# Kernel optimization log

Measured on AMD Instinct MI355X. Metric: run time of the kernel, lower is better.

Reference implementation:

```python
import jax, jax.numpy as jnp
import numpy as np

N = 20000        # genes
E = 100000       # edges per relation
D_IN = 512
HID = 64         # hidden_dim (per-head channels in layers 0,1)
HEADS = 8
D_H = HID * HEADS   # 512 hidden width
D_OUT = 256
NEG_SLOPE = 0.2  # GATv2Conv default negative_slope


def _gatv2(x, src, dst, Wl, bl, Wr, br, att, out_bias, heads, ch):
    """PyG GATv2Conv, add_self_loops=False, concat=True, eval mode (no dropout)."""
    n = x.shape[0]
    xl = (x @ Wl + bl).reshape(n, heads, ch)   # lin_l (source transform)
    xr = (x @ Wr + br).reshape(n, heads, ch)   # lin_r (target transform)
    e = jax.nn.leaky_relu(xl[src] + xr[dst], NEG_SLOPE)   # [E,H,C]
    score = jnp.einsum('ehc,hc->eh', e, att)              # [E,H]
    # segment softmax over incoming edges of each destination node
    m = jax.ops.segment_max(score, dst, num_segments=n)   # [N,H]
    w = jnp.exp(score - m[dst])
    z = jax.ops.segment_sum(w, dst, num_segments=n)
    alpha = w / z[dst]
    out = jax.ops.segment_sum(alpha[:, :, None] * xl[src], dst, num_segments=n)
    return out.reshape(n, heads * ch) + out_bias


def _layernorm(x, g, b):
    mu = x.mean(-1, keepdims=True)
    var = x.var(-1, keepdims=True)
    return (x - mu) * jax.lax.rsqrt(var + 1e-5) * g + b


def setup_inputs() -> dict:
    key = jax.random.key(0)
    ks = jax.random.split(key, 12)
    gn = lambda k, shape, fan_in: (jax.random.normal(k, shape, dtype=jnp.float32)
                                   / np.float32(np.sqrt(fan_in)))
    inp = {}
    inp['x'] = jax.random.normal(ks[0], (N, D_IN), dtype=jnp.float32)
    inp['edge_index'] = jax.random.randint(ks[1], (3, 2, E), 0, N, dtype=jnp.int32)
    # input projection  Linear(512 -> 512)
    inp['proj_w'] = gn(ks[2], (D_IN, D_H), D_IN)
    inp['proj_b'] = jnp.zeros((D_H,), jnp.float32)
    # layers 0,1: stacked over [layer, edge_type]
    inp['l01_lin_l_w'] = gn(ks[3], (2, 3, D_H, D_H), D_H)
    inp['l01_lin_l_b'] = jnp.zeros((2, 3, D_H), jnp.float32)
    inp['l01_lin_r_w'] = gn(ks[4], (2, 3, D_H, D_H), D_H)
    inp['l01_lin_r_b'] = jnp.zeros((2, 3, D_H), jnp.float32)
    inp['l01_att'] = gn(ks[5], (2, 3, HEADS, HID), HID)
    inp['l01_bias'] = jnp.zeros((2, 3, D_H), jnp.float32)
    # layer 2: heads=1, out_channels=256, stacked over edge_type
    inp['l2_lin_l_w'] = gn(ks[6], (3, D_H, D_OUT), D_H)
    inp['l2_lin_l_b'] = jnp.zeros((3, D_OUT), jnp.float32)
    inp['l2_lin_r_w'] = gn(ks[7], (3, D_H, D_OUT), D_H)
    inp['l2_lin_r_b'] = jnp.zeros((3, D_OUT), jnp.float32)
    inp['l2_att'] = gn(ks[8], (3, 1, D_OUT), D_OUT)
    inp['l2_bias'] = jnp.zeros((3, D_OUT), jnp.float32)
    # LayerNorms
    inp['ln01_gamma'] = jnp.ones((2, D_H), jnp.float32)
    inp['ln01_beta'] = jnp.zeros((2, D_H), jnp.float32)
    inp['ln2_gamma'] = jnp.ones((D_OUT,), jnp.float32)
    inp['ln2_beta'] = jnp.zeros((D_OUT,), jnp.float32)
    return inp


def reference(x, edge_index, proj_w, proj_b,
              l01_lin_l_w, l01_lin_l_b, l01_lin_r_w, l01_lin_r_b, l01_att, l01_bias,
              l2_lin_l_w, l2_lin_l_b, l2_lin_r_w, l2_lin_r_b, l2_att, l2_bias,
              ln01_gamma, ln01_beta, ln2_gamma, ln2_beta):
    # input proj + ELU (dropout = identity in eval)
    h = jax.nn.elu(x @ proj_w + proj_b)
    # layers 0 and 1: HeteroConv(sum over 3 relations), ELU, residual, LayerNorm
    for li in range(2):
        res = h
        out = 0.0
        for et in range(3):
            src, dst = edge_index[et, 0], edge_index[et, 1]
            out = out + _gatv2(h, src, dst,
                               l01_lin_l_w[li, et], l01_lin_l_b[li, et],
                               l01_lin_r_w[li, et], l01_lin_r_b[li, et],
                               l01_att[li, et], l01_bias[li, et], HEADS, HID)
        h = jax.nn.elu(out) + res
        h = _layernorm(h, ln01_gamma[li], ln01_beta[li])
    # layer 2: heads=1, out=256; no residual (dims differ)
    out = 0.0
    for et in range(3):
        src, dst = edge_index[et, 0], edge_index[et, 1]
        out = out + _gatv2(h, src, dst,
                           l2_lin_l_w[et], l2_lin_l_b[et],
                           l2_lin_r_w[et], l2_lin_r_b[et],
                           l2_att[et], l2_bias[et], 1, D_OUT)
    h = jax.nn.elu(out)
    return _layernorm(h, ln2_gamma, ln2_beta)
```

## Files before the change

### kernel.cpp

```cpp
#include <hip/hip_runtime.h>


#define NN 20000
#define NE 100000
#define DH 512
#define DOUT 256

typedef __attribute__((ext_vector_type(8))) short short8;
typedef __attribute__((ext_vector_type(4))) short short4v;
typedef __attribute__((ext_vector_type(4))) float f32x4;

__device__ __forceinline__ float b2f(unsigned short s) {
    union { unsigned u; float f; } v; v.u = ((unsigned)s) << 16; return v.f;
}
__device__ __forceinline__ unsigned short f2b(float f) {
    unsigned u = __float_as_uint(f);
    u += 0x7FFFu + ((u >> 16) & 1u);
    return (unsigned short)(u >> 16);
}
__device__ __forceinline__ void load_lds16(const unsigned short* g, unsigned short* l) {
    __builtin_amdgcn_global_load_lds(
        (const __attribute__((address_space(1))) unsigned int*)g,
        (__attribute__((address_space(3))) unsigned int*)l, 16, 0, 0);
}

__global__ void cvt_f2b_k(const float* __restrict__ in,
                          unsigned short* __restrict__ out, int n) {
    int i0 = (blockIdx.x * blockDim.x + threadIdx.x) * 8;
    if (i0 >= n) return;
    #pragma unroll
    for (int j = 0; j < 8; j++) out[i0 + j] = f2b(in[i0 + j]);
}

struct TSeg { const float* in; unsigned short* out; int C; };
struct TTable { TSeg s[19]; };

__global__ void transpose_all_k(TTable t) {
    __shared__ float tile[32][33];
    TSeg d = t.s[blockIdx.y];
    int tiles_x = d.C >> 5;
    int nt = tiles_x << 4;
    if ((int)blockIdx.x >= nt) return;
    int bx = blockIdx.x % tiles_x, by = blockIdx.x / tiles_x;
    int c0 = bx * 32, r0 = by * 32;
    int tx = threadIdx.x & 31, ty = threadIdx.x >> 5;
    #pragma unroll
    for (int i = ty; i < 32; i += 8)
        tile[i][tx] = d.in[(size_t)(r0 + i) * d.C + c0 + tx];
    __syncthreads();
    #pragma unroll
    for (int i = ty; i < 32; i += 8)
        d.out[(size_t)(c0 + i) * 512 + r0 + tx] = f2b(tile[tx][i]);
}

__global__ void count_all_k(const int* __restrict__ ei, int* __restrict__ counts) {
    int i = blockIdx.x * blockDim.x + threadIdx.x;
    if (i >= 3 * NE) return;
    int et = i / NE, idx = i - et * NE;
    int d = ei[(size_t)et * 2 * NE + NE + idx];
    atomicAdd(&counts[et * (NN + 1) + d], 1);
}

__global__ __launch_bounds__(1024)
void scan_par_k(const int* __restrict__ counts, int* __restrict__ offs, int n) {
    __shared__ int part[1024];
    const int* c = counts + (size_t)blockIdx.x * (n + 1);
    int* o = offs + (size_t)blockIdx.x * (n + 1);
    int tid = threadIdx.x;
    int per = (n + 1023) / 1024;
    int base = tid * per;
    int lim = min(base + per, n);
    int sum = 0;
    for (int i = base; i < lim; i++) sum += c[i];
    part[tid] = sum;
    __syncthreads();
    #pragma unroll
    for (int off = 1; off < 1024; off <<= 1) {
        int v = (tid >= off) ? part[tid - off] : 0;
        __syncthreads();
        part[tid] += v;
        __syncthreads();
    }
    int run = part[tid] - sum;
    for (int i = base; i < lim; i++) { o[i] = run; run += c[i]; }
    if (tid == 1023) o[n] = part[1023];
}

__global__ void scatter_all_k(const int* __restrict__ ei, int* __restrict__ cursor,
                              int* __restrict__ srcs_sorted) {
    int i = blockIdx.x * blockDim.x + threadIdx.x;
    if (i >= 3 * NE) return;
    int et = i / NE, idx = i - et * NE;
    int s = ei[(size_t)et * 2 * NE + idx];
    int d = ei[(size_t)et * 2 * NE + NE + idx];
    int p = atomicAdd(&cursor[et * (NN + 1) + d], 1);
    srcs_sorted[(size_t)et * NE + p] = s;
}

template<int ACT, int SEGL2>
__global__ __launch_bounds__(256)
void gemm_k(const unsigned short* __restrict__ A,
            const unsigned short* __restrict__ Bt,
            const float* __restrict__ lb,
            const float* __restrict__ rb,
            unsigned short* __restrict__ Cb,
            int M, int N, int K, int MT, int NT, int STRIPE) {
    __shared__ __align__(16) unsigned short smem[17408];
    unsigned short* As = smem;
    unsigned short* Bs = smem + 8192;
    int bid = blockIdx.x;
    int xcd = bid & 7, r = bid >> 3;
    int mtile = xcd * STRIPE + r / NT;
    int ntile = r % NT;
    if (mtile >= MT) return;
    int bm0 = mtile * 128, bn0 = ntile * 128;

    int tid = threadIdx.x;
    int lane = tid & 63, wave = tid >> 6;
    int quad = lane >> 4, l16 = lane & 15;
    int rw = (wave >> 1) * 64, cw = (wave & 1) * 64;
    int rxor = l16 & 7;

    f32x4 acc[4][4];
    #pragma unroll
    for (int mi = 0; mi < 4; mi++)
        #pragma unroll
        for (int ni = 0; ni < 4; ni++) acc[mi][ni] = (f32x4){0.f, 0.f, 0.f, 0.f};

    for (int k0 = 0; k0 < K; k0 += 64) {
        #pragma unroll
        for (int i = 0; i < 4; i++) {
            int f = i * 256 + tid;
            int row = f >> 3, s = f & 7;
            int cg = s ^ (row & 7);
            load_lds16(A + (size_t)(bm0 + row) * K + k0 + cg * 8, As + f * 8);
        }
        #pragma unroll
        for (int i = 0; i < 4; i++) {
            int f = i * 256 + tid;
            int col = f >> 3, s = f & 7;
            int cg = s ^ (col & 7);
            load_lds16(Bt + (size_t)(bn0 + col) * K + k0 + cg * 8, Bs + f * 8);
        }
        __syncthreads();
        #pragma unroll
        for (int ki = 0; ki < 64; ki += 32) {
            int kch = quad + (ki >> 3);
            int slot = kch ^ rxor;
            short8 af[4], bf[4];
            #pragma unroll
            for (int mi = 0; mi < 4; mi++)
                af[mi] = *(const short8*)(As + (rw + mi * 16 + l16) * 64 + slot * 8);
            #pragma unroll
            for (int ni = 0; ni < 4; ni++)
                bf[ni] = *(const short8*)(Bs + (cw + ni * 16 + l16) * 64 + slot * 8);
            #pragma unroll
            for (int mi = 0; mi < 4; mi++)
                #pragma unroll
                for (int ni = 0; ni < 4; ni++)
                    acc[mi][ni] = __builtin_amdgcn_mfma_f32_16x16x32_bf16(
                        af[mi], bf[ni], acc[mi][ni], 0, 0, 0);
        }
        __syncthreads();
    }

    #pragma unroll
    for (int ni = 0; ni < 4; ni++) {
        int col = cw + ni * 16 + l16;
        int seg = col >> (SEGL2 + 1);
        int lr = (col >> SEGL2) & 1;
        int cc2 = col & ((1 << SEGL2) - 1);
        float bv = (lr ? rb : lb)[(seg << SEGL2) + cc2];
        #pragma unroll
        for (int mi = 0; mi < 4; mi++) {
            int row = rw + mi * 16 + quad * 4;
            #pragma unroll
            for (int i = 0; i < 4; i++) {
                float v = acc[mi][ni][i] + bv;
                if (ACT == 1) v = v > 0.f ? v : expm1f(v);
                smem[(row + i) * 136 + col] = f2b(v);
            }
        }
    }
    __syncthreads();
    #pragma unroll
    for (int it = 0; it < 8; it++) {
        int chunk = it * 256 + tid;
        int row = chunk >> 4, cc = chunk & 15;
        int grow = bm0 + row;
        if (grow < M) {
            uint4 d = *(const uint4*)(smem + row * 136 + cc * 8);
            *(uint4*)(Cb + (size_t)grow * N + bn0 + cc * 8) = d;
        }
    }
}

__global__ __launch_bounds__(256)
void gat_fused01_k(const unsigned short* __restrict__ C,
                   const int* __restrict__ offs3,
                   const int* __restrict__ srcs3,
                   const float* __restrict__ att,
                   const float* __restrict__ bias3,
                   unsigned short* __restrict__ hb,
                   const float* __restrict__ gamma,
                   const float* __restrict__ beta,
                   int n_nodes) {
    const unsigned LD = 3072;
    __shared__ float red[4][2];
    int tid = threadIdx.x;
    int lane = tid & 63, wave = tid >> 6;
    int half = wave & 1;
    int n = blockIdx.x * 2 + (wave >> 1);
    int c0 = half * 256 + lane * 4;
    float tot[4] = {0.f, 0.f, 0.f, 0.f};

    #pragma unroll
    for (int et = 0; et < 3; et++) {
        const int* offs = offs3 + et * (NN + 1);
        const int* srcs = srcs3 + (size_t)et * NE;
        int e0 = offs[n], e1 = offs[n + 1];
        if (e0 == e1) continue;
        const unsigned short* XL = C + et * 1024 + c0;
        float xr[4], at[4];
        {
            short4v t = *(const short4v*)(C + (size_t)n * LD + et * 1024 + 512 + c0);
            #pragma unroll
            for (int j = 0; j < 4; j++) xr[j] = b2f((unsigned short)t[j]);
            #pragma unroll
            for (int j = 0; j < 4; j++) at[j] = att[et * 512 + c0 + j];
        }
        float z = 0.f, acc[4] = {0.f, 0.f, 0.f, 0.f};
        short4v p0 = *(const short4v*)(XL + (unsigned)srcs[e0] * LD);
        short4v p1 = (e0 + 1 < e1) ? *(const short4v*)(XL + (unsigned)srcs[e0 + 1] * LD) : p0;
        for (int e = e0; e < e1; e++) {
            short4v cur = p0;
            p0 = p1;
            if (e + 2 < e1) p1 = *(const short4v*)(XL + (unsigned)srcs[e + 2] * LD);
            float xl[4];
            #pragma unroll
            for (int j = 0; j < 4; j++) xl[j] = b2f((unsigned short)cur[j]);
            float p = 0.f;
            #pragma unroll
            for (int j = 0; j < 4; j++) {
                float v = xl[j] + xr[j];
                v = v > 0.f ? v : 0.2f * v;
                p += v * at[j];
            }
            p += __shfl_xor(p, 1, 64);
            p += __shfl_xor(p, 2, 64);
            p += __shfl_xor(p, 4, 64);
            p += __shfl_xor(p, 8, 64);
            float wgt = __expf(p);
            z += wgt;
            #pragma unroll
            for (int j = 0; j < 4; j++) acc[j] += wgt * xl[j];
        }
        float inv = 1.f / z;
        #pragma unroll
        for (int j = 0; j < 4; j++) tot[j] += acc[j] * inv;
    }

    unsigned short* hrow = hb + (size_t)n * DH + c0;
    float v[4]; float s1 = 0.f;
    {
        short4v rt = *(const short4v*)hrow;
        #pragma unroll
        for (int j = 0; j < 4; j++) {
            int c = c0 + j;
            float x = tot[j] + bias3[c] + bias3[512 + c] + bias3[1024 + c];
            x = x > 0.f ? x : expm1f(x);
            x += b2f((unsigned short)rt[j]);
            v[j] = x; s1 += x;
        }
    }
    #pragma unroll
    for (int off = 1; off < 64; off <<= 1) s1 += __shfl_xor(s1, off, 64);
    if (lane == 0) red[wave][0] = s1;
    __syncthreads();
    float s1full = s1 + red[wave ^ 1][0];
    float mean = s1full * (1.f / DH);
    float s2 = 0.f;
    #pragma unroll
    for (int j = 0; j < 4; j++) { float d = v[j] - mean; s2 += d * d; }
    #pragma unroll
    for (int off = 1; off < 64; off <<= 1) s2 += __shfl_xor(s2, off, 64);
    if (lane == 0) red[wave][1] = s2;
    __syncthreads();
    float s2full = s2 + red[wave ^ 1][1];
    float rstd = rsqrtf(s2full * (1.f / DH) + 1e-5f);
    unsigned short ov[4];
    #pragma unroll
    for (int j = 0; j < 4; j++) {
        int c = c0 + j;
        ov[j] = f2b((v[j] - mean) * rstd * gamma[c] + beta[c]);
    }
    *(short4v*)hrow = (short4v){(short)ov[0], (short)ov[1], (short)ov[2], (short)ov[3]};
}

__global__ void gat_fused2_k(const unsigned short* __restrict__ C,
                             const int* __restrict__ offs3,
                             const int* __restrict__ srcs3,
                             const float* __restrict__ att,
                             const float* __restrict__ bias3,
                             const float* __restrict__ gamma,
                             const float* __restrict__ beta,
                             float* __restrict__ out, int n_nodes) {
    const unsigned LD = 1536;
    int lane = threadIdx.x & 63;
    int n = blockIdx.x * (blockDim.x >> 6) + (threadIdx.x >> 6);
    if (n >= n_nodes) return;
    int c0 = lane * 4;
    float tot[4] = {0.f, 0.f, 0.f, 0.f};

    #pragma unroll
    for (int et = 0; et < 3; et++) {
        const int* offs = offs3 + et * (NN + 1);
        const int* srcs = srcs3 + (size_t)et * NE;
        int e0 = offs[n], e1 = offs[n + 1];
        if (e0 == e1) continue;
        const unsigned short* XL = C + et * 512 + c0;
        float xr[4], at[4];
        {
            short4v t = *(const short4v*)(C + (size_t)n * LD + et * 512 + 256 + c0);
            #pragma unroll
            for (int j = 0; j < 4; j++) xr[j] = b2f((unsigned short)t[j]);
            #pragma unroll
            for (int j = 0; j < 4; j++) at[j] = att[et * 256 + c0 + j];
        }
        float z = 0.f, acc[4] = {0.f, 0.f, 0.f, 0.f};
        short4v p0 = *(const short4v*)(XL + (unsigned)srcs[e0] * LD);
        short4v p1 = (e0 + 1 < e1) ? *(const short4v*)(XL + (unsigned)srcs[e0 + 1] * LD) : p0;
        for (int e = e0; e < e1; e++) {
            short4v cur = p0;
            p0 = p1;
            if (e + 2 < e1) p1 = *(const short4v*)(XL + (unsigned)srcs[e + 2] * LD);
            float xl[4];
            #pragma unroll
            for (int j = 0; j < 4; j++) xl[j] = b2f((unsigned short)cur[j]);
            float p = 0.f;
            #pragma unroll
            for (int j = 0; j < 4; j++) {
                float v = xl[j] + xr[j];
                v = v > 0.f ? v : 0.2f * v;
                p += v * at[j];
            }
            #pragma unroll
            for (int off = 1; off < 64; off <<= 1) p += __shfl_xor(p, off, 64);
            float wgt = __expf(p);
            z += wgt;
            #pragma unroll
            for (int j = 0; j < 4; j++) acc[j] += wgt * xl[j];
        }
        float inv = 1.f / z;
        #pragma unroll
        for (int j = 0; j < 4; j++) tot[j] += acc[j] * inv;
    }

    float v[4]; float s1 = 0.f;
    #pragma unroll
    for (int j = 0; j < 4; j++) {
        int c = c0 + j;
        float x = tot[j] + bias3[c] + bias3[256 + c] + bias3[512 + c];
        x = x > 0.f ? x : expm1f(x);
        v[j] = x; s1 += x;
    }
    #pragma unroll
    for (int off = 1; off < 64; off <<= 1) s1 += __shfl_xor(s1, off, 64);
    float mean = s1 * (1.f / DOUT);
    float s2 = 0.f;
    #pragma unroll
    for (int j = 0; j < 4; j++) { float d = v[j] - mean; s2 += d * d; }
    #pragma unroll
    for (int off = 1; off < 64; off <<= 1) s2 += __shfl_xor(s2, off, 64);
    float rstd = rsqrtf(s2 * (1.f / DOUT) + 1e-5f);
    #pragma unroll
    for (int j = 0; j < 4; j++) {
        int c = c0 + j;
        out[(size_t)n * DOUT + c] = (v[j] - mean) * rstd * gamma[c] + beta[c];
    }
}

extern "C" void kernel_launch(void* const* d_in, const int* in_sizes, int n_in,
                              void* d_out, int out_size, void* d_ws, size_t ws_size,
                              hipStream_t stream) {
    const float* x       = (const float*)d_in[0];
    const int*   ei      = (const int*)d_in[1];
    const float* proj_w  = (const float*)d_in[2];
    const float* proj_b  = (const float*)d_in[3];
    const float* l01lw   = (const float*)d_in[4];
    const float* l01lb   = (const float*)d_in[5];
    const float* l01rw   = (const float*)d_in[6];
    const float* l01rb   = (const float*)d_in[7];
    const float* l01att  = (const float*)d_in[8];
    const float* l01bias = (const float*)d_in[9];
    const float* l2lw    = (const float*)d_in[10];
    const float* l2lb    = (const float*)d_in[11];
    const float* l2rw    = (const float*)d_in[12];
    const float* l2rb    = (const float*)d_in[13];
    const float* l2att   = (const float*)d_in[14];
    const float* l2bias  = (const float*)d_in[15];
    const float* g01     = (const float*)d_in[16];
    const float* b01     = (const float*)d_in[17];
    const float* g2      = (const float*)d_in[18];
    const float* b2      = (const float*)d_in[19];
    (void)in_sizes; (void)n_in; (void)out_size; (void)ws_size;

    char* w = (char*)d_ws;
    size_t off = 0;
    auto carve = [&](size_t bytes) { void* p = w + off; off = (off + bytes + 255) & ~(size_t)255; return p; };
    unsigned short* h_b     = (unsigned short*)carve((size_t)NN * DH * 2);
    unsigned short* xb      = (unsigned short*)carve((size_t)NN * DH * 2);
    unsigned short* Cbuf    = (unsigned short*)carve((size_t)NN * 3072 * 2);
    unsigned short* Wt      = (unsigned short*)carve((size_t)4194304 * 2);
    int*            counts3 = (int*)           carve((size_t)3 * (NN + 1) * 4);
    int*            offs3   = (int*)           carve((size_t)3 * (NN + 1) * 4);
    int*            srcs3   = (int*)           carve((size_t)3 * NE * 4);
    carve(65536);

    unsigned short* Wt_proj = Wt;
    unsigned short* Wt_L0   = Wt_proj + 262144;
    unsigned short* Wt_L1   = Wt_L0 + 3072 * 512;
    unsigned short* Wt_L2   = Wt_L1 + 3072 * 512;

    dim3 tb(256);
    const int MT = (NN + 127) / 128;
    const int STRIPE = (MT + 7) / 8;

    cvt_f2b_k<<<dim3(5000), tb, 0, stream>>>(x, xb, NN * DH);
    TTable tt;
    {
        int s = 0;
        tt.s[s++] = {proj_w, Wt_proj, 512};
        for (int li = 0; li < 2; li++) {
            unsigned short* base = li ? Wt_L1 : Wt_L0;
            for (int et = 0; et < 3; et++)
                tt.s[s++] = {l01lw + (size_t)(li * 3 + et) * 262144,
                             base + (size_t)et * 2 * 262144, 512};
            for (int et = 0; et < 3; et++)
                tt.s[s++] = {l01rw + (size_t)(li * 3 + et) * 262144,
                             base + 262144 + (size_t)et * 2 * 262144, 512};
        }
        for (int et = 0; et < 3; et++)
            tt.s[s++] = {l2lw + (size_t)et * 131072,
                         Wt_L2 + (size_t)et * 2 * 131072, 256};
        for (int et = 0; et < 3; et++)
            tt.s[s++] = {l2rw + (size_t)et * 131072,
                         Wt_L2 + 131072 + (size_t)et * 2 * 131072, 256};
    }
    transpose_all_k<<<dim3(256, 19), tb, 0, stream>>>(tt);

    hipMemsetAsync(counts3, 0, (size_t)3 * (NN + 1) * 4, stream);
    count_all_k<<<dim3((3 * NE + 255) / 256), tb, 0, stream>>>(ei, counts3);
    scan_par_k<<<dim3(3), dim3(1024), 0, stream>>>(counts3, offs3, NN);
    hipMemcpyAsync(counts3, offs3, (size_t)3 * (NN + 1) * 4,
                   hipMemcpyDeviceToDevice, stream);
    scatter_all_k<<<dim3((3 * NE + 255) / 256), tb, 0, stream>>>(ei, counts3, srcs3);

    gemm_k<1, 9><<<dim3(8 * STRIPE * 4), tb, 0, stream>>>(
        xb, Wt_proj, proj_b, proj_b, h_b, NN, 512, 512, MT, 4, STRIPE);

    for (int li = 0; li < 2; li++) {
        gemm_k<0, 9><<<dim3(8 * STRIPE * 24), tb, 0, stream>>>(
            h_b, li ? Wt_L1 : Wt_L0,
            l01lb + (size_t)li * 3 * 512, l01rb + (size_t)li * 3 * 512,
            Cbuf, NN, 3072, 512, MT, 24, STRIPE);
        gat_fused01_k<<<dim3(NN / 2), tb, 0, stream>>>(
            Cbuf, offs3, srcs3,
            l01att + (size_t)li * 3 * 512, l01bias + (size_t)li * 3 * 512,
            h_b, g01 + (size_t)li * DH, b01 + (size_t)li * DH, NN);
    }

    gemm_k<0, 8><<<dim3(8 * STRIPE * 12), tb, 0, stream>>>(
        h_b, Wt_L2, l2lb, l2rb, Cbuf, NN, 1536, 512, MT, 12, STRIPE);
    gat_fused2_k<<<dim3(NN / 4), tb, 0, stream>>>(
        Cbuf, offs3, srcs3, l2att, l2bias, g2, b2, (float*)d_out, NN);
}
```

Before: 703.2 us.

## Parallelize GAT aggregation across edge types with one wave per relation

Both fused GAT kernels now launch one block per node with three waves, each handling one edge type in parallel instead of looping over the three relations sequentially. Partial sums from waves 1 and 2 go through shared memory and wave 0 does the bias, ELU, residual and LayerNorm. Layer 0/1 also widens each lane to 8 channels with 16-byte gathers, which cuts the head-reduction shuffles. The aim is more memory-level parallelism in the gather loop, at the cost of a block-wide sync, imbalance between relation degrees, and more, smaller blocks.

```diff
diff --git a/kernel.cpp b/kernel.cpp
--- a/kernel.cpp
+++ b/kernel.cpp
@@ -195,7 +195,7 @@
     }
 }
 
-__global__ __launch_bounds__(256)
+__global__ __launch_bounds__(192)
 void gat_fused01_k(const unsigned short* __restrict__ C,
                    const int* __restrict__ offs3,
                    const int* __restrict__ srcs3,
@@ -206,28 +206,131 @@
                    const float* __restrict__ beta,
                    int n_nodes) {
     const unsigned LD = 3072;
-    __shared__ float red[4][2];
+    __shared__ float lds_tot[2][DH];
     int tid = threadIdx.x;
-    int lane = tid & 63, wave = tid >> 6;
-    int half = wave & 1;
-    int n = blockIdx.x * 2 + (wave >> 1);
-    int c0 = half * 256 + lane * 4;
+    int lane = tid & 63, et = tid >> 6;
+    int n = blockIdx.x;
+    int c0 = lane * 8;
+
+    const int* offs = offs3 + et * (NN + 1);
+    const int* srcs = srcs3 + (size_t)et * NE;
+    int e0 = offs[n], e1 = offs[n + 1];
+
+    float tot[8];
+    #pragma unroll
+    for (int j = 0; j < 8; j++) tot[j] = 0.f;
+
+    if (e0 < e1) {
+        const unsigned short* XL = C + et * 1024 + c0;
+        float xr[8], at[8];
+        {
+            short8 t = *(const short8*)(C + (size_t)n * LD + et * 1024 + 512 + c0);
+            #pragma unroll
+            for (int j = 0; j < 8; j++) xr[j] = b2f((unsigned short)t[j]);
+            #pragma unroll
+            for (int j = 0; j < 8; j++) at[j] = att[et * 512 + c0 + j];
+        }
+        float z = 0.f, acc[8];
+        #pragma unroll
+        for (int j = 0; j < 8; j++) acc[j] = 0.f;
+        short8 p0 = *(const short8*)(XL + (unsigned)srcs[e0] * LD);
+        short8 p1 = (e0 + 1 < e1) ? *(const short8*)(XL + (unsigned)srcs[e0 + 1] * LD) : p0;
+        for (int e = e0; e < e1; e++) {
+            short8 cur = p0;
+            p0 = p1;
+            if (e + 2 < e1) p1 = *(const short8*)(XL + (unsigned)srcs[e + 2] * LD);
+            float xl[8];
+            #pragma unroll
+            for (int j = 0; j < 8; j++) xl[j] = b2f((unsigned short)cur[j]);
+            float p = 0.f;
+            #pragma unroll
+            for (int j = 0; j < 8; j++) {
+                float v = xl[j] + xr[j];
+                v = fmaxf(v, 0.2f * v);
+                p = fmaf(v, at[j], p);
+            }
+            p += __shfl_xor(p, 1, 64);
+            p += __shfl_xor(p, 2, 64);
+            p += __shfl_xor(p, 4, 64);
+            float wgt = __expf(p);
+            z += wgt;
+            #pragma unroll
+            for (int j = 0; j < 8; j++) acc[j] = fmaf(wgt, xl[j], acc[j]);
+        }
+        float inv = 1.f / z;
+        #pragma unroll
+        for (int j = 0; j < 8; j++) tot[j] = acc[j] * inv;
+    }
+
+    if (et) {
+        #pragma unroll
+        for (int j = 0; j < 8; j++) lds_tot[et - 1][c0 + j] = tot[j];
+    }
+    __syncthreads();
+    if (et == 0) {
+        unsigned short* hrow = hb + (size_t)n * DH + c0;
+        short8 rt = *(const short8*)hrow;
+        float v[8]; float s1 = 0.f;
+        #pragma unroll
+        for (int j = 0; j < 8; j++) {
+            int c = c0 + j;
+            float x = tot[j] + lds_tot[0][c] + lds_tot[1][c]
+                    + bias3[c] + bias3[512 + c] + bias3[1024 + c];
+            x = x > 0.f ? x : expm1f(x);
+            x += b2f((unsigned short)rt[j]);
+            v[j] = x; s1 += x;
+        }
+        #pragma unroll
+        for (int off = 1; off < 64; off <<= 1) s1 += __shfl_xor(s1, off, 64);
+        float mean = s1 * (1.f / DH);
+        float s2 = 0.f;
+        #pragma unroll
+        for (int j = 0; j < 8; j++) { float d = v[j] - mean; s2 += d * d; }
+        #pragma unroll
+        for (int off = 1; off < 64; off <<= 1) s2 += __shfl_xor(s2, off, 64);
+        float rstd = rsqrtf(s2 * (1.f / DH) + 1e-5f);
+        short8 ov;
+        #pragma unroll
+        for (int j = 0; j < 8; j++) {
+            int c = c0 + j;
+            ov[j] = (short)f2b((v[j] - mean) * rstd * gamma[c] + beta[c]);
+        }
+        *(short8*)hrow = ov;
+    }
+    (void)n_nodes;
+}
+
+__global__ __launch_bounds__(192)
+void gat_fused2_k(const unsigned short* __restrict__ C,
+                  const int* __restrict__ offs3,
+                  const int* __restrict__ srcs3,
+                  const float* __restrict__ att,
+                  const float* __restrict__ bias3,
+                  const float* __restrict__ gamma,
+                  const float* __restrict__ beta,
+                  float* __restrict__ out, int n_nodes) {
+    const unsigned LD = 1536;
+    __shared__ float lds_tot[2][DOUT];
+    int tid = threadIdx.x;
+    int lane = tid & 63, et = tid >> 6;
+    int n = blockIdx.x;
+    int c0 = lane * 4;
+
+    const int* offs = offs3 + et * (NN + 1);
+    const int* srcs = srcs3 + (size_t)et * NE;
+    int e0 = offs[n], e1 = offs[n + 1];
+
     float tot[4] = {0.f, 0.f, 0.f, 0.f};
 
-    #pragma unroll
-    for (int et = 0; et < 3; et++) {
-        const int* offs = offs3 + et * (NN + 1);
-        const int* srcs = srcs3 + (size_t)et * NE;
-        int e0 = offs[n], e1 = offs[n + 1];
-        if (e0 == e1) continue;
-        const unsigned short* XL = C + et * 1024 + c0;
+    if (e0 < e1) {
+        const unsigned short* XL = C + et * 512 + c0;
         float xr[4], at[4];
         {
-            short4v t = *(const short4v*)(C + (size_t)n * LD + et * 1024 + 512 + c0);
+            short4v t = *(const short4v*)(C + (size_t)n * LD + et * 512 + 256 + c0);
             #pragma unroll
             for (int j = 0; j < 4; j++) xr[j] = b2f((unsigned short)t[j]);
             #pragma unroll
-            for (int j = 0; j < 4; j++) at[j] = att[et * 512 + c0 + j];
+            for (int j = 0; j < 4; j++) at[j] = att[et * 256 + c0 + j];
         }
         float z = 0.f, acc[4] = {0.f, 0.f, 0.f, 0.f};
         short4v p0 = *(const short4v*)(XL + (unsigned)srcs[e0] * LD);
@@ -243,141 +346,54 @@
             #pragma unroll
             for (int j = 0; j < 4; j++) {
                 float v = xl[j] + xr[j];
-                v = v > 0.f ? v : 0.2f * v;
-                p += v * at[j];
-            }
-            p += __shfl_xor(p, 1, 64);
-            p += __shfl_xor(p, 2, 64);
-            p += __shfl_xor(p, 4, 64);
-            p += __shfl_xor(p, 8, 64);
-            float wgt = __expf(p);
-            z += wgt;
-            #pragma unroll
-            for (int j = 0; j < 4; j++) acc[j] += wgt * xl[j];
-        }
-        float inv = 1.f / z;
-        #pragma unroll
-        for (int j = 0; j < 4; j++) tot[j] += acc[j] * inv;
-    }
-
-    unsigned short* hrow = hb + (size_t)n * DH + c0;
-    float v[4]; float s1 = 0.f;
-    {
-        short4v rt = *(const short4v*)hrow;
-        #pragma unroll
-        for (int j = 0; j < 4; j++) {
-            int c = c0 + j;
-            float x = tot[j] + bias3[c] + bias3[512 + c] + bias3[1024 + c];
-            x = x > 0.f ? x : expm1f(x);
-            x += b2f((unsigned short)rt[j]);
-            v[j] = x; s1 += x;
-        }
-    }
-    #pragma unroll
-    for (int off = 1; off < 64; off <<= 1) s1 += __shfl_xor(s1, off, 64);
-    if (lane == 0) red[wave][0] = s1;
-    __syncthreads();
-    float s1full = s1 + red[wave ^ 1][0];
-    float mean = s1full * (1.f / DH);
-    float s2 = 0.f;
-    #pragma unroll
-    for (int j = 0; j < 4; j++) { float d = v[j] - mean; s2 += d * d; }
-    #pragma unroll
-    for (int off = 1; off < 64; off <<= 1) s2 += __shfl_xor(s2, off, 64);
-    if (lane == 0) red[wave][1] = s2;
-    __syncthreads();
-    float s2full = s2 + red[wave ^ 1][1];
-    float rstd = rsqrtf(s2full * (1.f / DH) + 1e-5f);
-    unsigned short ov[4];
-    #pragma unroll
-    for (int j = 0; j < 4; j++) {
-        int c = c0 + j;
-        ov[j] = f2b((v[j] - mean) * rstd * gamma[c] + beta[c]);
-    }
-    *(short4v*)hrow = (short4v){(short)ov[0], (short)ov[1], (short)ov[2], (short)ov[3]};
-}
-
-__global__ void gat_fused2_k(const unsigned short* __restrict__ C,
-                             const int* __restrict__ offs3,
-                             const int* __restrict__ srcs3,
-                             const float* __restrict__ att,
-                             const float* __restrict__ bias3,
-                             const float* __restrict__ gamma,
-                             const float* __restrict__ beta,
-                             float* __restrict__ out, int n_nodes) {
-    const unsigned LD = 1536;
-    int lane = threadIdx.x & 63;
-    int n = blockIdx.x * (blockDim.x >> 6) + (threadIdx.x >> 6);
-    if (n >= n_nodes) return;
-    int c0 = lane * 4;
-    float tot[4] = {0.f, 0.f, 0.f, 0.f};
-
-    #pragma unroll
-    for (int et = 0; et < 3; et++) {
-        const int* offs = offs3 + et * (NN + 1);
-        const int* srcs = srcs3 + (size_t)et * NE;
-        int e0 = offs[n], e1 = offs[n + 1];
-        if (e0 == e1) continue;
-        const unsigned short* XL = C + et * 512 + c0;
-        float xr[4], at[4];
-        {
-            short4v t = *(const short4v*)(C + (size_t)n * LD + et * 512 + 256 + c0);
-            #pragma unroll
-            for (int j = 0; j < 4; j++) xr[j] = b2f((unsigned short)t[j]);
-            #pragma unroll
-            for (int j = 0; j < 4; j++) at[j] = att[et * 256 + c0 + j];
-        }
-        float z = 0.f, acc[4] = {0.f, 0.f, 0.f, 0.f};
-        short4v p0 = *(const short4v*)(XL + (unsigned)srcs[e0] * LD);
-        short4v p1 = (e0 + 1 < e1) ? *(const short4v*)(XL + (unsigned)srcs[e0 + 1] * LD) : p0;
-        for (int e = e0; e < e1; e++) {
-            short4v cur = p0;
-            p0 = p1;
-            if (e + 2 < e1) p1 = *(const short4v*)(XL + (unsigned)srcs[e + 2] * LD);
-            float xl[4];
-            #pragma unroll
-            for (int j = 0; j < 4; j++) xl[j] = b2f((unsigned short)cur[j]);
-            float p = 0.f;
-            #pragma unroll
-            for (int j = 0; j < 4; j++) {
-                float v = xl[j] + xr[j];
-                v = v > 0.f ? v : 0.2f * v;
-                p += v * at[j];
+                v = fmaxf(v, 0.2f * v);
+                p = fmaf(v, at[j], p);
             }
             #pragma unroll
             for (int off = 1; off < 64; off <<= 1) p += __shfl_xor(p, off, 64);
             float wgt = __expf(p);
             z += wgt;
             #pragma unroll
-            for (int j = 0; j < 4; j++) acc[j] += wgt * xl[j];
+            for (int j = 0; j < 4; j++) acc[j] = fmaf(wgt, xl[j], acc[j]);
         }
         float inv = 1.f / z;
         #pragma unroll
-        for (int j = 0; j < 4; j++) tot[j] += acc[j] * inv;
-    }
-
-    float v[4]; float s1 = 0.f;
-    #pragma unroll
-    for (int j = 0; j < 4; j++) {
-        int c = c0 + j;
-        float x = tot[j] + bias3[c] + bias3[256 + c] + bias3[512 + c];
-        x = x > 0.f ? x : expm1f(x);
-        v[j] = x; s1 += x;
-    }
-    #pragma unroll
-    for (int off = 1; off < 64; off <<= 1) s1 += __shfl_xor(s1, off, 64);
-    float mean = s1 * (1.f / DOUT);
-    float s2 = 0.f;
-    #pragma unroll
-    for (int j = 0; j < 4; j++) { float d = v[j] - mean; s2 += d * d; }
-    #pragma unroll
-    for (int off = 1; off < 64; off <<= 1) s2 += __shfl_xor(s2, off, 64);
-    float rstd = rsqrtf(s2 * (1.f / DOUT) + 1e-5f);
-    #pragma unroll
-    for (int j = 0; j < 4; j++) {
-        int c = c0 + j;
-        out[(size_t)n * DOUT + c] = (v[j] - mean) * rstd * gamma[c] + beta[c];
-    }
+        for (int j = 0; j < 4; j++) tot[j] = acc[j] * inv;
+    }
+
+    if (et) {
+        #pragma unroll
+        for (int j = 0; j < 4; j++) lds_tot[et - 1][c0 + j] = tot[j];
+    }
+    __syncthreads();
+    if (et == 0) {
+        float v[4]; float s1 = 0.f;
+        #pragma unroll
+        for (int j = 0; j < 4; j++) {
+            int c = c0 + j;
+            float x = tot[j] + lds_tot[0][c] + lds_tot[1][c]
+                    + bias3[c] + bias3[256 + c] + bias3[512 + c];
+            x = x > 0.f ? x : expm1f(x);
+            v[j] = x; s1 += x;
+        }
+        #pragma unroll
+        for (int off = 1; off < 64; off <<= 1) s1 += __shfl_xor(s1, off, 64);
+        float mean = s1 * (1.f / DOUT);
+        float s2 = 0.f;
+        #pragma unroll
+        for (int j = 0; j < 4; j++) { float d = v[j] - mean; s2 += d * d; }
+        #pragma unroll
+        for (int off = 1; off < 64; off <<= 1) s2 += __shfl_xor(s2, off, 64);
+        float rstd = rsqrtf(s2 * (1.f / DOUT) + 1e-5f);
+        f32x4 o;
+        #pragma unroll
+        for (int j = 0; j < 4; j++) {
+            int c = c0 + j;
+            o[j] = (v[j] - mean) * rstd * gamma[c] + beta[c];
+        }
+        *(f32x4*)(out + (size_t)n * DOUT + c0) = o;
+    }
+    (void)n_nodes;
 }
 
 extern "C" void kernel_launch(void* const* d_in, const int* in_sizes, int n_in,
@@ -464,7 +480,7 @@
             h_b, li ? Wt_L1 : Wt_L0,
             l01lb + (size_t)li * 3 * 512, l01rb + (size_t)li * 3 * 512,
             Cbuf, NN, 3072, 512, MT, 24, STRIPE);
-        gat_fused01_k<<<dim3(NN / 2), tb, 0, stream>>>(
+        gat_fused01_k<<<dim3(NN), dim3(192), 0, stream>>>(
             Cbuf, offs3, srcs3,
             l01att + (size_t)li * 3 * 512, l01bias + (size_t)li * 3 * 512,
             h_b, g01 + (size_t)li * DH, b01 + (size_t)li * DH, NN);
@@ -472,6 +488,6 @@
 
     gemm_k<0, 8><<<dim3(8 * STRIPE * 12), tb, 0, stream>>>(
         h_b, Wt_L2, l2lb, l2rb, Cbuf, NN, 1536, 512, MT, 12, STRIPE);
-    gat_fused2_k<<<dim3(NN / 4), tb, 0, stream>>>(
+    gat_fused2_k<<<dim3(NN), dim3(192), 0, stream>>>(
         Cbuf, offs3, srcs3, l2att, l2bias, g2, b2, (float*)d_out, NN);
 }
```

Result: faster. 649.5 us (-7.6%).
